# Kernel optimization log

Measured on AMD Instinct MI355X. Metric: run time of the kernel, lower is better.

## Reference

```python
import jax, jax.numpy as jnp
import numpy as np

N = 32          # agents_num
IN_DIM = 16     # node feature dim (excluding 2 pos cols)
HID = 128
HEADS = 4
OUT = 5
DUEL_H = 256
RADIUS = 0.3
LATENT = HID + HID * HEADS * 2  # 1152
BS = 128


def _lin(k, i, o):
    s = 1.0 / np.sqrt(i)
    return jax.random.uniform(k, (i, o), minval=-s, maxval=s, dtype=jnp.float32)


def setup_inputs() -> dict:
    key = jax.random.key(0)
    ks = jax.random.split(key, 16)
    pos = jax.random.uniform(ks[0], (BS, N, 2))
    feats = jax.random.normal(ks[1], (BS, N, IN_DIM))
    aidx = jax.random.randint(ks[2], (BS,), 0, N).astype(jnp.float32)
    node = jnp.concatenate([pos, feats], axis=-1).reshape(BS, N * (2 + IN_DIM))
    obs = jnp.concatenate([node, aidx[:, None]], axis=1)  # (BS, N*(2+IN_DIM)+1)
    return {
        "obs": obs,
        "enc_w1": _lin(ks[3], IN_DIM, HID), "enc_b1": jnp.zeros((HID,)),
        "enc_w2": _lin(ks[4], HID, HID), "enc_b2": jnp.zeros((HID,)),
        "wl1": _lin(ks[5], HID, HEADS * HID), "wr1": _lin(ks[6], HID, HEADS * HID),
        "att1": jax.random.normal(ks[7], (HEADS, HID)) * 0.1, "bias1": jnp.zeros((HEADS * HID,)),
        "wl2": _lin(ks[8], HID * HEADS, HEADS * HID), "wr2": _lin(ks[9], HID * HEADS, HEADS * HID),
        "att2": jax.random.normal(ks[10], (HEADS, HID)) * 0.1, "bias2": jnp.zeros((HEADS * HID,)),
        "q_w1": _lin(ks[11], LATENT, DUEL_H), "q_b1": jnp.zeros((DUEL_H,)),
        "q_w2": _lin(ks[12], DUEL_H, OUT), "q_b2": jnp.zeros((OUT,)),
        "v_w1": _lin(ks[13], LATENT, DUEL_H), "v_b1": jnp.zeros((DUEL_H,)),
        "v_w2": _lin(ks[14], DUEL_H, 1), "v_b2": jnp.zeros((1,)),
    }


def _gatv2(x, adj, wl, wr, att, bias):
    # Dense-masked GATv2 (PyG semantics: lin_l on source j, lin_r on target i,
    # leaky_relu(x_i + x_j) . att, softmax over neighbors j, aggregate lin_l(x_j)).
    bs, n, _ = x.shape
    gl = (x @ wl).reshape(bs, n, HEADS, HID)  # source transform
    gr = (x @ wr).reshape(bs, n, HEADS, HID)  # target transform
    e = jax.nn.leaky_relu(gr[:, :, None] + gl[:, None, :], 0.2)  # [b, i, j, h, c]
    logits = jnp.einsum('bijhc,hc->bijh', e, att)
    logits = jnp.where(adj[..., None], logits, -jnp.inf)  # diag always True (self loops)
    alpha = jax.nn.softmax(logits, axis=2)
    out = jnp.einsum('bijh,bjhc->bihc', alpha, gl).reshape(bs, n, HEADS * HID)
    return out + bias


def reference(obs, enc_w1, enc_b1, enc_w2, enc_b2,
              wl1, wr1, att1, bias1, wl2, wr2, att2, bias2,
              q_w1, q_b1, q_w2, q_b2, v_w1, v_b1, v_w2, v_b2):
    bs = obs.shape[0]
    node = obs[:, :-1].reshape(bs, N, 2 + IN_DIM)
    pos, feats = node[..., :2], node[..., 2:]
    aidx = jnp.clip(obs[:, -1], 0, N - 1).astype(jnp.int32)

    # radius_graph (per-graph, loop=False) + GATv2 add_self_loops => diag True
    d2 = jnp.sum((pos[:, :, None] - pos[:, None, :]) ** 2, axis=-1)  # [bs, N, N]
    adj = (d2 < RADIUS ** 2) | jnp.eye(N, dtype=bool)

    # encoder MLP then ReLU (as in forward)
    h = jax.nn.relu(feats @ enc_w1 + enc_b1)
    x = jax.nn.relu(h @ enc_w2 + enc_b2)  # [bs, N, HID]

    b = jnp.arange(bs)
    x1 = x[b, aidx]  # [bs, HID]

    x = jax.nn.relu(_gatv2(x, adj, wl1, wr1, att1, bias1))  # [bs, N, HID*HEADS]
    x2 = x[b, aidx]

    x = jax.nn.relu(_gatv2(x, adj, wl2, wr2, att2, bias2))
    x3 = x[b, aidx]

    x_cat = jnp.concatenate([x1, x2, x3], axis=1)  # [bs, LATENT]

    q = jax.nn.relu(x_cat @ q_w1 + q_b1) @ q_w2 + q_b2  # [bs, OUT]
    v = jax.nn.relu(x_cat @ v_w1 + v_b1) @ v_w2 + v_b2  # [bs, 1]
    return q - q.mean(axis=1, keepdims=True) + v
```

## Files before the change

kernel.cpp:

```cpp
#include <hip/hip_runtime.h>
#include <hip/hip_bf16.h>

typedef unsigned int uint_t;
typedef unsigned short ushort_t;
typedef __attribute__((ext_vector_type(8))) short short8;
typedef __attribute__((ext_vector_type(4))) float floatx4;

__device__ __forceinline__ float4 fma4(float4 a, float s, float4 w){
  a.x += s*w.x; a.y += s*w.y; a.z += s*w.z; a.w += s*w.w; return a;
}
__device__ __forceinline__ float4 relu4(float4 a){
  return make_float4(fmaxf(a.x,0.f),fmaxf(a.y,0.f),fmaxf(a.z,0.f),fmaxf(a.w,0.f));
}
__device__ __forceinline__ unsigned bf16rne(float f){
  unsigned u = __float_as_uint(f);
  return (u + 0x7fffu + ((u>>16)&1u)) >> 16;
}
__device__ __forceinline__ uint_t packbf(float f){
  unsigned hb = bf16rne(f);
  float hf = __uint_as_float(hb<<16);
  unsigned lb = bf16rne(f - hf);
  return (hb<<16) | lb;
}
__device__ __forceinline__ uint4 pack4(float4 v){
  uint4 u; u.x=packbf(v.x); u.y=packbf(v.y); u.z=packbf(v.z); u.w=packbf(v.w); return u;
}
__device__ __forceinline__ float unpk(uint_t u){
  return __uint_as_float(u & 0xffff0000u) + __uint_as_float(u<<16);
}
#define UNPACK8(u0,u1,hi,lo) \
  hi[0]=(short)(u0.x>>16); lo[0]=(short)u0.x; \
  hi[1]=(short)(u0.y>>16); lo[1]=(short)u0.y; \
  hi[2]=(short)(u0.z>>16); lo[2]=(short)u0.z; \
  hi[3]=(short)(u0.w>>16); lo[3]=(short)u0.w; \
  hi[4]=(short)(u1.x>>16); lo[4]=(short)u1.x; \
  hi[5]=(short)(u1.y>>16); lo[5]=(short)u1.y; \
  hi[6]=(short)(u1.z>>16); lo[6]=(short)u1.z; \
  hi[7]=(short)(u1.w>>16); lo[7]=(short)u1.w;


__device__ __forceinline__ void hgemm_body(
    const uint_t* __restrict__ xcatpk,
    const ushort_t* __restrict__ qw1Thi, const ushort_t* __restrict__ qw1Tlo,
    const ushort_t* __restrict__ vw1Thi, const ushort_t* __restrict__ vw1Tlo,
    float* __restrict__ part, int ks, int ct, int t)
{
  const int w = t>>6, lane = t&63, m = lane&15, quad = lane>>4;
  const ushort_t* Bhi = (ct<4) ? qw1Thi : vw1Thi;
  const ushort_t* Blo = (ct<4) ? qw1Tlo : vw1Tlo;
  const int cbl = (ct<4) ? ct*64 : (ct-4)*64;
  const int cbg = (ct<4) ? ct*64 : 256 + (ct-4)*64;
  const uint_t* ap = xcatpk + (size_t)w*18432 + m*32 + quad*8 + (size_t)(ks*6)*512;
  const ushort_t* bp0 = Bhi + (size_t)((cbl>>4)+0)*18432 + m*32 + quad*8 + (size_t)(ks*6)*512;
  const ushort_t* bp1 = Bhi + (size_t)((cbl>>4)+1)*18432 + m*32 + quad*8 + (size_t)(ks*6)*512;
  const ushort_t* bp2 = Bhi + (size_t)((cbl>>4)+2)*18432 + m*32 + quad*8 + (size_t)(ks*6)*512;
  const ushort_t* bp3 = Bhi + (size_t)((cbl>>4)+3)*18432 + m*32 + quad*8 + (size_t)(ks*6)*512;
  const size_t lod = (size_t)(qw1Tlo - qw1Thi);
  floatx4 acc[4];
  #pragma unroll
  for (int i=0;i<4;i++) acc[i] = (floatx4){0.f,0.f,0.f,0.f};
  #pragma unroll
  for (int kc=0; kc<6; kc++){
    const uint4 ua0 = *(const uint4*)(ap);
    const uint4 ua1 = *(const uint4*)(ap+4);
    ap += 512;
    short8 ahi, alo;
    UNPACK8(ua0,ua1,ahi,alo)
    const ushort_t* bps[4] = {bp0, bp1, bp2, bp3};
    #pragma unroll
    for (int nt=0; nt<4; nt++){
      const short8 bh = *(const short8*)(bps[nt] + kc*512);
      const short8 bl = *(const short8*)(bps[nt] + kc*512 + lod);
      acc[nt] = __builtin_amdgcn_mfma_f32_16x16x32_bf16(ahi, bh, acc[nt], 0,0,0);
      acc[nt] = __builtin_amdgcn_mfma_f32_16x16x32_bf16(ahi, bl, acc[nt], 0,0,0);
      acc[nt] = __builtin_amdgcn_mfma_f32_16x16x32_bf16(alo, bh, acc[nt], 0,0,0);
    }
  }
  float* pdst = part + (size_t)ks*65536;
  const int crow0 = w*16 + quad*4;
  #pragma unroll
  for (int nt=0; nt<4; nt++){
    const int col = cbg + nt*16 + m;
    #pragma unroll
    for (int r=0;r<4;r++)
      pdst[(size_t)(crow0 + r)*512 + col] = acc[nt][r];
  }
}

__global__ __launch_bounds__(256) void prep_kernel(
    const float* __restrict__ obs,
    const float* __restrict__ enc_w1, const float* __restrict__ enc_b1,
    const float* __restrict__ enc_w2, const float* __restrict__ enc_b2,
    const float* __restrict__ wl1, const float* __restrict__ wr1,
    ushort_t* __restrict__ wl1Thi, ushort_t* __restrict__ wl1Tlo,
    ushort_t* __restrict__ wr1Thi, ushort_t* __restrict__ wr1Tlo,
    uint_t* __restrict__ xpk, uint_t* __restrict__ xcatpk,
    unsigned* __restrict__ adjw, int* __restrict__ aiw)
{
  const int t = threadIdx.x, bid = blockIdx.x;
  if (bid >= 512){
    __shared__ float sm[32][33];
    const int cw = bid - 512;
    const float* in; ushort_t* ohi; ushort_t* olo; int tt;
    const int K = 128, N = 512;
    if (cw < 64){ in=wl1; ohi=wl1Thi; olo=wl1Tlo; tt=cw; }
    else        { in=wr1; ohi=wr1Thi; olo=wr1Tlo; tt=cw-64; }
    const int ktiles = K>>5;
    const int kt = tt % ktiles, nt = tt / ktiles;
    const int r = t>>5, c = t&31;
    #pragma unroll
    for (int i=0;i<4;i++)
      sm[r+i*8][c] = in[(size_t)(kt*32 + r + i*8)*N + nt*32 + c];
    __syncthreads();
    #pragma unroll
    for (int i=0;i<4;i++){
      const int nl = r + i*8;
      const int n  = nt*32 + nl;
      const float f = sm[c][nl];
      const unsigned hb = bf16rne(f);
      const float hf = __uint_as_float(hb<<16);
      const unsigned lb = bf16rne(f - hf);
      const size_t off = (size_t)(n>>4)*(16*K) + (size_t)kt*512 + (size_t)(n&15)*32 + c;
      ohi[off] = (ushort_t)hb;
      olo[off] = (ushort_t)lb;
    }
    return;
  }
  __shared__ float s_pos[64];
  __shared__ float s_feats[128];
  __shared__ __align__(16) float s_h[8*132];
  __shared__ int s_ai;
  const int s = bid>>2, g = bid&3;
  const float* ob = obs + s*577;

  if (t==0){
    float a = ob[576];
    a = fminf(fmaxf(a, 0.f), 31.f);
    s_ai = (int)a;
    if (g==0) aiw[s] = (int)a;
  }
  if (t < 128){ const int n=t>>4, f=t&15; s_feats[t] = ob[(g*8+n)*18+2+f]; }
  if (g==0 && t>=128 && t<192){ const int u=t-128; s_pos[u] = ob[(u>>1)*18 + (u&1)]; }
  __syncthreads();

  if (g==0 && t < 32){
    const float px = s_pos[2*t], py = s_pos[2*t+1];
    const float R2 = 0.09f;
    unsigned mm = 0u;
    for (int j=0;j<32;j++){
      const float dx = __fsub_rn(px, s_pos[2*j]), dy = __fsub_rn(py, s_pos[2*j+1]);
      const float d2 = __fadd_rn(__fmul_rn(dx,dx), __fmul_rn(dy,dy));
      if (d2 <= R2 || j==t) mm |= (1u<<j);
    }
    adjw[s*32+t] = mm;
  }

  const int n = t>>5, c0 = (t&31)*4;
  {
    float4 a = *(const float4*)(enc_b1+c0);
    #pragma unroll
    for (int f=0; f<16; f++)
      a = fma4(a, s_feats[n*16+f], *(const float4*)(enc_w1 + f*128 + c0));
    *(float4*)&s_h[n*132+c0] = relu4(a);
  }
  __syncthreads();
  {
    float4 a = *(const float4*)(enc_b2+c0);
    for (int k=0;k<128;k+=4){
      const float4 hv = *(const float4*)&s_h[n*132+k];
      a = fma4(a, hv.x, *(const float4*)(enc_w2 + (k+0)*128 + c0));
      a = fma4(a, hv.y, *(const float4*)(enc_w2 + (k+1)*128 + c0));
      a = fma4(a, hv.z, *(const float4*)(enc_w2 + (k+2)*128 + c0));
      a = fma4(a, hv.w, *(const float4*)(enc_w2 + (k+3)*128 + c0));
    }
    a = relu4(a);
    const uint4 p = pack4(a);
    const int i = g*8 + n;
    uint_t* xp = xpk + (size_t)(s*2 + (i>>4))*2048 + (c0>>5)*512 + (i&15)*32 + (c0&31);
    *(uint4*)xp = p;
    if (i == s_ai){
      uint_t* xc = xcatpk + (size_t)(s>>4)*18432 + (c0>>5)*512 + (s&15)*32 + (c0&31);
      *(uint4*)xc = p;
    }
  }
}

__global__ __launch_bounds__(512) void pa1_kernel(
    const uint_t* __restrict__ xpk,
    const ushort_t* __restrict__ wl1Thi, const ushort_t* __restrict__ wl1Tlo,
    const ushort_t* __restrict__ wr1Thi, const ushort_t* __restrict__ wr1Tlo,
    const float* __restrict__ att, const float* __restrict__ bias,
    const unsigned* __restrict__ adjw, const int* __restrict__ aiw,
    const float* __restrict__ wl2, const float* __restrict__ q_w1, const float* __restrict__ v_w1,
    ushort_t* __restrict__ wl2Thi, ushort_t* __restrict__ wl2Tlo,
    ushort_t* __restrict__ qw1Thi, ushort_t* __restrict__ qw1Tlo,
    ushort_t* __restrict__ vw1Thi, ushort_t* __restrict__ vw1Tlo,
    uint_t* __restrict__ x2pk, uint_t* __restrict__ xcatpk)
{
  __shared__ __align__(16) float s_gl[32*132];
  __shared__ __align__(16) float s_glB[32*132];
  __shared__ __align__(16) float s_gr[32*132];
  __shared__ __align__(16) float s_grB[32*132];
  __shared__ __align__(16) float s_att[128];
  __shared__ __align__(16) float s_b[128];
  __shared__ float s_lg[32*33];
  __shared__ unsigned s_adj[32];
  const int t = threadIdx.x, bid = blockIdx.x;

  if (bid >= 512){
    const int cw = bid - 512;
    const float* in; ushort_t* ohi; ushort_t* olo; int K, N, tt;
    if (cw < 256)      { in=wl2;  ohi=wl2Thi; olo=wl2Tlo; K=512;  N=512; tt=cw; }
    else if (cw < 544) { in=q_w1; ohi=qw1Thi; olo=qw1Tlo; K=1152; N=256; tt=cw-256; }
    else               { in=v_w1; ohi=vw1Thi; olo=vw1Tlo; K=1152; N=256; tt=cw-544; }
    const int ktiles = K>>5;
    const int kt = tt % ktiles, nt = tt / ktiles;
    const int r = t>>5, c = t&31;
    #pragma unroll
    for (int i=0;i<2;i++)
      s_gl[(r+i*16)*33 + c] = in[(size_t)(kt*32 + r + i*16)*N + nt*32 + c];
    __syncthreads();
    #pragma unroll
    for (int i=0;i<2;i++){
      const int nl = r + i*16;
      const int n  = nt*32 + nl;
      const float f = s_gl[c*33 + nl];
      const unsigned hb = bf16rne(f);
      const float hf = __uint_as_float(hb<<16);
      const unsigned lb = bf16rne(f - hf);
      const size_t off = (size_t)(n>>4)*(16*K) + (size_t)kt*512 + (size_t)(n&15)*32 + c;
      ohi[off] = (ushort_t)hb;
      olo[off] = (ushort_t)lb;
    }
    return;
  }

  const int s = bid >> 2, h = bid & 3;
  const int w = t>>6, lane = t&63, m = lane&15, quad = lane>>4;
  const int ww = w&3, khalf = w>>2;

  if (t < 128){ s_att[t] = att[h*128 + t]; s_b[t] = bias[h*128 + t]; }
  if (t >= 224 && t < 256) s_adj[t-224] = adjw[s*32 + (t-224)];
  const int ai = aiw[s];

  const ushort_t* Bhi = (ww<2) ? wl1Thi : wr1Thi;
  const ushort_t* Blo = (ww<2) ? wl1Tlo : wr1Tlo;
  const int nbase = h*8 + (ww&1)*4;
  const int kcb = khalf*2;
  const uint_t* a0p = xpk + (size_t)(s*2+0)*2048 + m*32 + quad*8 + kcb*512;
  const uint_t* a1p = xpk + (size_t)(s*2+1)*2048 + m*32 + quad*8 + kcb*512;
  const ushort_t* bp0 = Bhi + (size_t)(nbase+0)*2048 + m*32 + quad*8 + kcb*512;
  const ushort_t* bp1 = Bhi + (size_t)(nbase+1)*2048 + m*32 + quad*8 + kcb*512;
  const ushort_t* bp2 = Bhi + (size_t)(nbase+2)*2048 + m*32 + quad*8 + kcb*512;
  const ushort_t* bp3 = Bhi + (size_t)(nbase+3)*2048 + m*32 + quad*8 + kcb*512;
  const size_t lod = (size_t)(Blo - Bhi);
  floatx4 acc[2][4];
  #pragma unroll
  for (int i=0;i<2;i++)
    #pragma unroll
    for (int j=0;j<4;j++) acc[i][j] = (floatx4){0.f,0.f,0.f,0.f};

  #pragma unroll
  for (int kc=0; kc<2; kc++){
    const uint4 u00 = *(const uint4*)(a0p + kc*512);
    const uint4 u01 = *(const uint4*)(a0p + kc*512 + 4);
    const uint4 u10 = *(const uint4*)(a1p + kc*512);
    const uint4 u11 = *(const uint4*)(a1p + kc*512 + 4);
    short8 ahi0, alo0, ahi1, alo1;
    UNPACK8(u00,u01,ahi0,alo0)
    UNPACK8(u10,u11,ahi1,alo1)
    const ushort_t* bps[4] = {bp0, bp1, bp2, bp3};
    #pragma unroll
    for (int nt=0; nt<4; nt++){
      const short8 bh = *(const short8*)(bps[nt] + kc*512);
      const short8 bl = *(const short8*)(bps[nt] + kc*512 + lod);
      acc[0][nt] = __builtin_amdgcn_mfma_f32_16x16x32_bf16(ahi0, bh, acc[0][nt], 0,0,0);
      acc[0][nt] = __builtin_amdgcn_mfma_f32_16x16x32_bf16(ahi0, bl, acc[0][nt], 0,0,0);
      acc[0][nt] = __builtin_amdgcn_mfma_f32_16x16x32_bf16(alo0, bh, acc[0][nt], 0,0,0);
      acc[1][nt] = __builtin_amdgcn_mfma_f32_16x16x32_bf16(ahi1, bh, acc[1][nt], 0,0,0);
      acc[1][nt] = __builtin_amdgcn_mfma_f32_16x16x32_bf16(ahi1, bl, acc[1][nt], 0,0,0);
      acc[1][nt] = __builtin_amdgcn_mfma_f32_16x16x32_bf16(alo1, bh, acc[1][nt], 0,0,0);
    }
  }
  {
    float* dst = (ww<2) ? (khalf ? s_glB : s_gl) : (khalf ? s_grB : s_gr);
    const int colbase = (ww&1)*64;
    #pragma unroll
    for (int nt=0; nt<4; nt++){
      const int col = colbase + nt*16 + m;
      #pragma unroll
      for (int r=0;r<4;r++){
        dst[(quad*4+r)*132 + col]      = acc[0][nt][r];
        dst[(16+quad*4+r)*132 + col]   = acc[1][nt][r];
      }
    }
  }
  __syncthreads();
  for (int e=t; e<32*132; e+=512){
    s_gl[e] += s_glB[e];
    s_gr[e] += s_grB[e];
  }
  __syncthreads();

  {
    const int i = t>>4, jb = t&15;
    float lacc[2] = {0.f,0.f};
    for (int c=0;c<128;c+=4){
      const float4 g = *(const float4*)&s_gr[i*132+c];
      const float4 a = *(const float4*)&s_att[c];
      #pragma unroll
      for (int mm=0;mm<2;mm++){
        const float4 gj = *(const float4*)&s_gl[(jb+16*mm)*132 + c];
        float ex = g.x+gj.x; ex = fmaxf(ex, 0.2f*ex);
        float ey = g.y+gj.y; ey = fmaxf(ey, 0.2f*ey);
        float ez = g.z+gj.z; ez = fmaxf(ez, 0.2f*ez);
        float ew = g.w+gj.w; ew = fmaxf(ew, 0.2f*ew);
        lacc[mm] += ex*a.x + ey*a.y + ez*a.z + ew*a.w;
      }
    }
    s_lg[i*33 + jb]      = lacc[0];
    s_lg[i*33 + jb + 16] = lacc[1];
  }
  __syncthreads();

  #pragma unroll
  for (int rnd=0; rnd<2; rnd++){
    const int i = rnd*16 + (t>>5), j = t&31;
    const float lg = s_lg[i*33+j];
    const bool ok = (s_adj[i]>>j)&1u;
    float v = ok ? lg : -3.0e38f;
    #pragma unroll
    for (int d_=16; d_; d_>>=1) v = fmaxf(v, __shfl_xor(v, d_, 32));
    const float e = ok ? __expf(lg - v) : 0.f;
    float sum = e;
    #pragma unroll
    for (int d_=16; d_; d_>>=1) sum += __shfl_xor(sum, d_, 32);
    s_lg[i*33+j] = e / sum;
  }
  __syncthreads();

  {
    const int i = t>>4, c0 = (t&15)*8;
    float4 o0 = make_float4(0.f,0.f,0.f,0.f), o1 = o0;
    for (int j=0;j<32;j++){
      const float al = s_lg[i*33+j];
      o0 = fma4(o0, al, *(const float4*)&s_gl[j*132 + c0]);
      o1 = fma4(o1, al, *(const float4*)&s_gl[j*132 + c0 + 4]);
    }
    const float4 b0 = *(const float4*)&s_b[c0];
    const float4 b1 = *(const float4*)&s_b[c0+4];
    o0 = relu4(make_float4(o0.x+b0.x, o0.y+b0.y, o0.z+b0.z, o0.w+b0.w));
    o1 = relu4(make_float4(o1.x+b1.x, o1.y+b1.y, o1.z+b1.z, o1.w+b1.w));
    const uint4 p0 = pack4(o0), p1 = pack4(o1);
    const int kb = h*128 + c0;
    uint_t* xp = x2pk + (size_t)(s*2 + (i>>4))*8192 + (kb>>5)*512 + (i&15)*32 + (kb&31);
    *(uint4*)&xp[0] = p0;
    *(uint4*)&xp[4] = p1;
    if (i == ai){
      const int kk = 128 + kb;
      uint_t* tp = xcatpk + (size_t)(s>>4)*18432 + (kk>>5)*512 + (s&15)*32 + (kk&31);
      *(uint4*)&tp[0] = p0;
      *(uint4*)&tp[4] = p1;
    }
  }
}

__global__ __launch_bounds__(512) void pa2_kernel(
    const uint_t* __restrict__ x2pk,
    const ushort_t* __restrict__ wl2Thi, const ushort_t* __restrict__ wl2Tlo,
    const float* __restrict__ wr2f,
    const float* __restrict__ att2, const float* __restrict__ bias2,
    const unsigned* __restrict__ adjw, const int* __restrict__ aiw,
    const ushort_t* __restrict__ qw1Thi, const ushort_t* __restrict__ qw1Tlo,
    const ushort_t* __restrict__ vw1Thi, const ushort_t* __restrict__ vw1Tlo,
    float* __restrict__ hpart,
    uint_t* __restrict__ xcatpk)
{
  const int t = threadIdx.x, bid = blockIdx.x;
  if (bid >= 512){
    const int hk = bid - 512;
    hgemm_body(xcatpk, qw1Thi, qw1Tlo, vw1Thi, vw1Tlo, hpart, hk>>3, hk&7, t);
    return;
  }
  __shared__ __align__(16) float s_gl[32*132];
  __shared__ __align__(16) float s_glB[32*132];
  __shared__ __align__(16) float s_xt[512];
  __shared__ __align__(16) float s_p2[4*128];
  __shared__ __align__(16) float s_at[128];
  __shared__ __align__(16) float s_bb[128];
  __shared__ float s_lg[32];
  __shared__ float s_al[32];
  const int s = bid >> 2, h = bid & 3;
  const int w = t>>6, lane = t&63, m = lane&15, quad = lane>>4;
  const int ww = w&3, khalf = w>>2;
  const int ai = aiw[s];
  const unsigned arow = adjw[s*32+ai];

  {
    const int kk = 128 + t;
    s_xt[t] = unpk(xcatpk[(size_t)(s>>4)*18432 + (kk>>5)*512 + (s&15)*32 + (kk&31)]);
  }
  if (t < 128){ s_at[t] = att2[h*128+t]; s_bb[t] = bias2[h*128+t]; }
  __syncthreads();

  {
    const int c = t&127, q4 = t>>7;
    const float* wp = wr2f + (size_t)(q4*128)*512 + h*128 + c;
    float ga = 0.f;
    #pragma unroll 8
    for (int k=0;k<128;k++) ga += s_xt[q4*128 + k] * wp[(size_t)k*512];
    s_p2[q4*128 + c] = ga;
  }

  const int kcb = khalf*8;
  const uint_t* a0p = x2pk + (size_t)(s*2+0)*8192 + m*32 + quad*8 + kcb*512;
  const uint_t* a1p = x2pk + (size_t)(s*2+1)*8192 + m*32 + quad*8 + kcb*512;
  const ushort_t* bq0 = wl2Thi + (size_t)(h*8 + ww*2+0)*8192 + m*32 + quad*8 + kcb*512;
  const ushort_t* bq1 = wl2Thi + (size_t)(h*8 + ww*2+1)*8192 + m*32 + quad*8 + kcb*512;
  const size_t lod = (size_t)(wl2Tlo - wl2Thi);
  floatx4 acc[2][2];
  #pragma unroll
  for (int i=0;i<2;i++){ acc[i][0] = (floatx4){0.f,0.f,0.f,0.f}; acc[i][1] = acc[i][0]; }
  #pragma unroll 4
  for (int kc=0; kc<8; kc++){
    const uint4 u00 = *(const uint4*)(a0p + kc*512);
    const uint4 u01 = *(const uint4*)(a0p + kc*512 + 4);
    const uint4 u10 = *(const uint4*)(a1p + kc*512);
    const uint4 u11 = *(const uint4*)(a1p + kc*512 + 4);
    short8 ahi0, alo0, ahi1, alo1;
    UNPACK8(u00,u01,ahi0,alo0)
    UNPACK8(u10,u11,ahi1,alo1)
    {
      const short8 bh = *(const short8*)(bq0 + kc*512);
      const short8 bl = *(const short8*)(bq0 + kc*512 + lod);
      acc[0][0] = __builtin_amdgcn_mfma_f32_16x16x32_bf16(ahi0, bh, acc[0][0], 0,0,0);
      acc[0][0] = __builtin_amdgcn_mfma_f32_16x16x32_bf16(ahi0, bl, acc[0][0], 0,0,0);
      acc[0][0] = __builtin_amdgcn_mfma_f32_16x16x32_bf16(alo0, bh, acc[0][0], 0,0,0);
      acc[1][0] = __builtin_amdgcn_mfma_f32_16x16x32_bf16(ahi1, bh, acc[1][0], 0,0,0);
      acc[1][0] = __builtin_amdgcn_mfma_f32_16x16x32_bf16(ahi1, bl, acc[1][0], 0,0,0);
      acc[1][0] = __builtin_amdgcn_mfma_f32_16x16x32_bf16(alo1, bh, acc[1][0], 0,0,0);
    }
    {
      const short8 bh = *(const short8*)(bq1 + kc*512);
      const short8 bl = *(const short8*)(bq1 + kc*512 + lod);
      acc[0][1] = __builtin_amdgcn_mfma_f32_16x16x32_bf16(ahi0, bh, acc[0][1], 0,0,0);
      acc[0][1] = __builtin_amdgcn_mfma_f32_16x16x32_bf16(ahi0, bl, acc[0][1], 0,0,0);
      acc[0][1] = __builtin_amdgcn_mfma_f32_16x16x32_bf16(alo0, bh, acc[0][1], 0,0,0);
      acc[1][1] = __builtin_amdgcn_mfma_f32_16x16x32_bf16(ahi1, bh, acc[1][1], 0,0,0);
      acc[1][1] = __builtin_amdgcn_mfma_f32_16x16x32_bf16(ahi1, bl, acc[1][1], 0,0,0);
      acc[1][1] = __builtin_amdgcn_mfma_f32_16x16x32_bf16(alo1, bh, acc[1][1], 0,0,0);
    }
  }
  {
    float* dst = khalf ? s_glB : s_gl;
    const int colbase = ww*32;
    #pragma unroll
    for (int nt=0; nt<2; nt++){
      const int col = colbase + nt*16 + m;
      #pragma unroll
      for (int r=0;r<4;r++){
        dst[(quad*4+r)*132 + col]    = acc[0][nt][r];
        dst[(16+quad*4+r)*132 + col] = acc[1][nt][r];
      }
    }
  }
  __syncthreads();
  for (int e=t; e<32*132; e+=512) s_gl[e] += s_glB[e];
  if (t < 128) s_p2[t] = s_p2[t] + s_p2[128+t] + s_p2[256+t] + s_p2[384+t];
  __syncthreads();

  if (t < 256){
    const int j = t>>3, pq = t&7;
    float sum = 0.f;
    #pragma unroll
    for (int q=0;q<4;q++){
      const int c = pq*16 + q*4;
      const float4 g = *(const float4*)&s_gl[j*132 + c];
      const float4 r = *(const float4*)&s_p2[c];
      const float4 a = *(const float4*)&s_at[c];
      float e0 = r.x+g.x; e0 = fmaxf(e0, 0.2f*e0);
      float e1 = r.y+g.y; e1 = fmaxf(e1, 0.2f*e1);
      float e2 = r.z+g.z; e2 = fmaxf(e2, 0.2f*e2);
      float e3 = r.w+g.w; e3 = fmaxf(e3, 0.2f*e3);
      sum += e0*a.x + e1*a.y + e2*a.z + e3*a.w;
    }
    sum += __shfl_xor(sum,1,64);
    sum += __shfl_xor(sum,2,64);
    sum += __shfl_xor(sum,4,64);
    if (pq==0) s_lg[j] = sum;
  }
  __syncthreads();
  if (t < 32){
    const float lg = s_lg[t];
    const bool ok = (arow>>t)&1u;
    float v = ok ? lg : -3.0e38f;
    #pragma unroll
    for (int d_=16; d_; d_>>=1) v = fmaxf(v, __shfl_xor(v, d_, 32));
    const float e = ok ? __expf(lg - v) : 0.f;
    float sm = e;
    #pragma unroll
    for (int d_=16; d_; d_>>=1) sm += __shfl_xor(sm, d_, 32);
    s_al[t] = e / sm;
  }
  __syncthreads();
  if (t < 128){
    float acc2 = 0.f;
    #pragma unroll 8
    for (int j=0;j<32;j++) acc2 += s_al[j] * s_gl[j*132 + t];
    const int kk = 640 + h*128 + t;
    xcatpk[(size_t)(s>>4)*18432 + (kk>>5)*512 + (s&15)*32 + (kk&31)]
        = packbf(fmaxf(acc2 + s_bb[t], 0.f));
  }
}

__global__ __launch_bounds__(512) void hgemm_kernel(
    const uint_t* __restrict__ xcatpk,
    const ushort_t* __restrict__ qw1Thi, const ushort_t* __restrict__ qw1Tlo,
    const ushort_t* __restrict__ vw1Thi, const ushort_t* __restrict__ vw1Tlo,
    float* __restrict__ hpart)
{
  const int t = threadIdx.x, bid = blockIdx.x;
  hgemm_body(xcatpk, qw1Thi, qw1Tlo, vw1Thi, vw1Tlo, hpart, 3 + (bid>>3), bid&7, t);
}

__global__ __launch_bounds__(256) void hepi_kernel(
    const float* __restrict__ hpart,
    const float* __restrict__ q_b1, const float* __restrict__ q_w2, const float* __restrict__ q_b2,
    const float* __restrict__ v_b1, const float* __restrict__ v_w2, const float* __restrict__ v_b2,
    float* __restrict__ out)
{
  __shared__ float s_p[4*6];
  const int t = threadIdx.x, s = blockIdx.x;
  float hq = q_b1[t], hv = v_b1[t];
  #pragma unroll
  for (int ks=0; ks<6; ks++){
    hq += hpart[(size_t)ks*65536 + (size_t)s*512 + t];
    hv += hpart[(size_t)ks*65536 + (size_t)s*512 + 256 + t];
  }
  hq = fmaxf(hq, 0.f);
  hv = fmaxf(hv, 0.f);
  float p[6];
  #pragma unroll
  for (int o=0;o<5;o++) p[o] = hq * q_w2[t*5+o];
  p[5] = hv * v_w2[t];
  #pragma unroll
  for (int d_=32; d_; d_>>=1){
    #pragma unroll
    for (int o=0;o<6;o++) p[o] += __shfl_xor(p[o], d_, 64);
  }
  const int w = t>>6, lane = t&63;
  if (lane==0){
    #pragma unroll
    for (int o=0;o<6;o++) s_p[w*6+o] = p[o];
  }
  __syncthreads();
  if (t < 6) s_p[t] = s_p[t] + s_p[6+t] + s_p[12+t] + s_p[18+t];
  __syncthreads();
  if (t < 5){
    const float q0 = s_p[0]+q_b2[0], q1 = s_p[1]+q_b2[1], q2 = s_p[2]+q_b2[2],
                q3 = s_p[3]+q_b2[3], q4 = s_p[4]+q_b2[4];
    const float mean = (q0+q1+q2+q3+q4) / 5.0f;
    const float v = s_p[5] + v_b2[0];
    const float qt = (t==0?q0:t==1?q1:t==2?q2:t==3?q3:q4);
    out[s*5+t] = qt - mean + v;
  }
}

extern "C" void kernel_launch(void* const* d_in, const int* in_sizes, int n_in,
                              void* d_out, int out_size, void* d_ws, size_t ws_size,
                              hipStream_t stream) {
  (void)n_in; (void)out_size; (void)ws_size;
  const float* obs    = (const float*)d_in[0];
  const float* enc_w1 = (const float*)d_in[1];
  const float* enc_b1 = (const float*)d_in[2];
  const float* enc_w2 = (const float*)d_in[3];
  const float* enc_b2 = (const float*)d_in[4];
  const float* wl1    = (const float*)d_in[5];
  const float* wr1    = (const float*)d_in[6];
  const float* att1   = (const float*)d_in[7];
  const float* bias1  = (const float*)d_in[8];
  const float* wl2    = (const float*)d_in[9];
  const float* wr2    = (const float*)d_in[10];
  const float* att2   = (const float*)d_in[11];
  const float* bias2  = (const float*)d_in[12];
  const float* q_w1   = (const float*)d_in[13];
  const float* q_b1   = (const float*)d_in[14];
  const float* q_w2   = (const float*)d_in[15];
  const float* q_b2   = (const float*)d_in[16];
  const float* v_w1   = (const float*)d_in[17];
  const float* v_b1   = (const float*)d_in[18];
  const float* v_w2   = (const float*)d_in[19];
  const float* v_b2   = (const float*)d_in[20];

  char* ws = (char*)d_ws;
  uint_t*   x_pk    = (uint_t*)  (ws + 0);
  uint_t*   xcat_pk = (uint_t*)  (ws + 2097152);
  unsigned* adjw    = (unsigned*)(ws + 2686976);
  int*      aiw     = (int*)     (ws + 2703360);
  uint_t*   x2_pk   = (uint_t*)  (ws + 2703872);
  ushort_t* wl1Thi  = (ushort_t*)(ws + 11092480);
  ushort_t* wl1Tlo  = (ushort_t*)(ws + 11223552);
  ushort_t* wr1Thi  = (ushort_t*)(ws + 11354624);
  ushort_t* wr1Tlo  = (ushort_t*)(ws + 11485696);
  ushort_t* wl2Thi  = (ushort_t*)(ws + 11616768);
  ushort_t* wl2Tlo  = (ushort_t*)(ws + 12141056);
  ushort_t* qw1Thi  = (ushort_t*)(ws + 12665344);
  ushort_t* qw1Tlo  = (ushort_t*)(ws + 13255168);
  ushort_t* vw1Thi  = (ushort_t*)(ws + 13844992);
  ushort_t* vw1Tlo  = (ushort_t*)(ws + 14434816);
  float*    hpart   = (float*)   (ws + 15024640);

  const int bs = in_sizes[0] / 577;

  prep_kernel<<<512 + 128, 256, 0, stream>>>(obs, enc_w1, enc_b1, enc_w2, enc_b2,
      wl1, wr1, wl1Thi, wl1Tlo, wr1Thi, wr1Tlo,
      x_pk, xcat_pk, adjw, aiw);

  pa1_kernel<<<512 + 832, 512, 0, stream>>>(x_pk, wl1Thi, wl1Tlo, wr1Thi, wr1Tlo,
      att1, bias1, adjw, aiw,
      wl2, q_w1, v_w1, wl2Thi, wl2Tlo, qw1Thi, qw1Tlo, vw1Thi, vw1Tlo,
      x2_pk, xcat_pk);

  pa2_kernel<<<512 + 24, 512, 0, stream>>>(x2_pk, wl2Thi, wl2Tlo, wr2,
      att2, bias2, adjw, aiw,
      qw1Thi, qw1Tlo, vw1Thi, vw1Tlo, hpart, xcat_pk);

  hgemm_kernel<<<24, 512, 0, stream>>>(xcat_pk, qw1Thi, qw1Tlo, vw1Thi, vw1Tlo, hpart);

  hepi_kernel<<<bs, 256, 0, stream>>>(hpart, q_b1, q_w2, q_b2, v_b1, v_w2, v_b2,
                                      (float*)d_out);
}
```

Measured before the change: 181.2 us.

## Fuse x3 slice of dueling-head GEMM into GAT layer-2 kernel, drop hgemm launch

The x3 slice of the dueling-head first-layer GEMM now runs inside the GAT layer-2 attention blocks. Each block multiplies its freshly computed 128-wide head output by the matching fp32 q_w1/v_w1 rows and writes a per-head partial to a new buffer. The remaining K range (x1,x2) is re-split into 4 chunks of 5 k-tiles handled by the 32 side blocks, and the separate hgemm kernel launch is removed. This removes a launch and a serialization point in exchange for scalar fp32 GEMV work in every attention block, strided global weight reads, and an extra partial buffer that the epilogue must sum.

```diff
diff --git a/kernel.cpp b/kernel.cpp
--- a/kernel.cpp
+++ b/kernel.cpp
@@ -47,20 +47,19 @@
 {
   const int w = t>>6, lane = t&63, m = lane&15, quad = lane>>4;
   const ushort_t* Bhi = (ct<4) ? qw1Thi : vw1Thi;
-  const ushort_t* Blo = (ct<4) ? qw1Tlo : vw1Tlo;
   const int cbl = (ct<4) ? ct*64 : (ct-4)*64;
   const int cbg = (ct<4) ? ct*64 : 256 + (ct-4)*64;
-  const uint_t* ap = xcatpk + (size_t)w*18432 + m*32 + quad*8 + (size_t)(ks*6)*512;
-  const ushort_t* bp0 = Bhi + (size_t)((cbl>>4)+0)*18432 + m*32 + quad*8 + (size_t)(ks*6)*512;
-  const ushort_t* bp1 = Bhi + (size_t)((cbl>>4)+1)*18432 + m*32 + quad*8 + (size_t)(ks*6)*512;
-  const ushort_t* bp2 = Bhi + (size_t)((cbl>>4)+2)*18432 + m*32 + quad*8 + (size_t)(ks*6)*512;
-  const ushort_t* bp3 = Bhi + (size_t)((cbl>>4)+3)*18432 + m*32 + quad*8 + (size_t)(ks*6)*512;
+  const uint_t* ap = xcatpk + (size_t)w*18432 + m*32 + quad*8 + (size_t)(ks*5)*512;
+  const ushort_t* bp0 = Bhi + (size_t)((cbl>>4)+0)*18432 + m*32 + quad*8 + (size_t)(ks*5)*512;
+  const ushort_t* bp1 = Bhi + (size_t)((cbl>>4)+1)*18432 + m*32 + quad*8 + (size_t)(ks*5)*512;
+  const ushort_t* bp2 = Bhi + (size_t)((cbl>>4)+2)*18432 + m*32 + quad*8 + (size_t)(ks*5)*512;
+  const ushort_t* bp3 = Bhi + (size_t)((cbl>>4)+3)*18432 + m*32 + quad*8 + (size_t)(ks*5)*512;
   const size_t lod = (size_t)(qw1Tlo - qw1Thi);
   floatx4 acc[4];
   #pragma unroll
   for (int i=0;i<4;i++) acc[i] = (floatx4){0.f,0.f,0.f,0.f};
   #pragma unroll
-  for (int kc=0; kc<6; kc++){
+  for (int kc=0; kc<5; kc++){
     const uint4 ua0 = *(const uint4*)(ap);
     const uint4 ua1 = *(const uint4*)(ap+4);
     ap += 512;
@@ -373,7 +372,8 @@
     const unsigned* __restrict__ adjw, const int* __restrict__ aiw,
     const ushort_t* __restrict__ qw1Thi, const ushort_t* __restrict__ qw1Tlo,
     const ushort_t* __restrict__ vw1Thi, const ushort_t* __restrict__ vw1Tlo,
-    float* __restrict__ hpart,
+    const float* __restrict__ q_w1f, const float* __restrict__ v_w1f,
+    float* __restrict__ hpart, float* __restrict__ hp3,
     uint_t* __restrict__ xcatpk)
 {
   const int t = threadIdx.x, bid = blockIdx.x;
@@ -507,24 +507,27 @@
     float acc2 = 0.f;
     #pragma unroll 8
     for (int j=0;j<32;j++) acc2 += s_al[j] * s_gl[j*132 + t];
+    const float x3v = fmaxf(acc2 + s_bb[t], 0.f);
     const int kk = 640 + h*128 + t;
-    xcatpk[(size_t)(s>>4)*18432 + (kk>>5)*512 + (s&15)*32 + (kk&31)]
-        = packbf(fmaxf(acc2 + s_bb[t], 0.f));
-  }
-}
-
-__global__ __launch_bounds__(512) void hgemm_kernel(
-    const uint_t* __restrict__ xcatpk,
-    const ushort_t* __restrict__ qw1Thi, const ushort_t* __restrict__ qw1Tlo,
-    const ushort_t* __restrict__ vw1Thi, const ushort_t* __restrict__ vw1Tlo,
-    float* __restrict__ hpart)
-{
-  const int t = threadIdx.x, bid = blockIdx.x;
-  hgemm_body(xcatpk, qw1Thi, qw1Tlo, vw1Thi, vw1Tlo, hpart, 3 + (bid>>3), bid&7, t);
+    xcatpk[(size_t)(s>>4)*18432 + (kk>>5)*512 + (s&15)*32 + (kk&31)] = packbf(x3v);
+    s_xt[t] = x3v;
+  }
+  __syncthreads();
+
+  {
+    const float* W; int col;
+    if (t < 256){ W = q_w1f; col = t; }
+    else        { W = v_w1f; col = t-256; }
+    const float* wp = W + (size_t)(640 + h*128)*256 + col;
+    float acc3 = 0.f;
+    #pragma unroll 8
+    for (int k=0;k<128;k++) acc3 += s_xt[k] * wp[(size_t)k*256];
+    hp3[((size_t)h*128 + s)*512 + t] = acc3;
+  }
 }
 
 __global__ __launch_bounds__(256) void hepi_kernel(
-    const float* __restrict__ hpart,
+    const float* __restrict__ hpart, const float* __restrict__ hp3,
     const float* __restrict__ q_b1, const float* __restrict__ q_w2, const float* __restrict__ q_b2,
     const float* __restrict__ v_b1, const float* __restrict__ v_w2, const float* __restrict__ v_b2,
     float* __restrict__ out)
@@ -533,9 +536,14 @@
   const int t = threadIdx.x, s = blockIdx.x;
   float hq = q_b1[t], hv = v_b1[t];
   #pragma unroll
-  for (int ks=0; ks<6; ks++){
+  for (int ks=0; ks<4; ks++){
     hq += hpart[(size_t)ks*65536 + (size_t)s*512 + t];
     hv += hpart[(size_t)ks*65536 + (size_t)s*512 + 256 + t];
+  }
+  #pragma unroll
+  for (int h=0; h<4; h++){
+    hq += hp3[((size_t)h*128 + s)*512 + t];
+    hv += hp3[((size_t)h*128 + s)*512 + 256 + t];
   }
   hq = fmaxf(hq, 0.f);
   hv = fmaxf(hv, 0.f);
@@ -609,6 +617,7 @@
   ushort_t* vw1Thi  = (ushort_t*)(ws + 13844992);
   ushort_t* vw1Tlo  = (ushort_t*)(ws + 14434816);
   float*    hpart   = (float*)   (ws + 15024640);
+  float*    hp3     = (float*)   (ws + 16073216);
 
   const int bs = in_sizes[0] / 577;
 
@@ -621,12 +630,10 @@
       wl2, q_w1, v_w1, wl2Thi, wl2Tlo, qw1Thi, qw1Tlo, vw1Thi, vw1Tlo,
       x2_pk, xcat_pk);
 
-  pa2_kernel<<<512 + 24, 512, 0, stream>>>(x2_pk, wl2Thi, wl2Tlo, wr2,
+  pa2_kernel<<<512 + 32, 512, 0, stream>>>(x2_pk, wl2Thi, wl2Tlo, wr2,
       att2, bias2, adjw, aiw,
-      qw1Thi, qw1Tlo, vw1Thi, vw1Tlo, hpart, xcat_pk);
-
-  hgemm_kernel<<<24, 512, 0, stream>>>(xcat_pk, qw1Thi, qw1Tlo, vw1Thi, vw1Tlo, hpart);
-
-  hepi_kernel<<<bs, 256, 0, stream>>>(hpart, q_b1, q_w2, q_b2, v_b1, v_w2, v_b2,
+      qw1Thi, qw1Tlo, vw1Thi, vw1Tlo, q_w1, v_w1, hpart, hp3, xcat_pk);
+
+  hepi_kernel<<<bs, 256, 0, stream>>>(hpart, hp3, q_b1, q_w2, q_b2, v_b1, v_w2, v_b2,
                                       (float*)d_out);
 }
```

Measured after the change: 175.6 us. 3.1% less time.
